# Kernel tuning notes

Hardware: AMD Instinct MI355X
Metric: run time of the kernel (lower is better)

## Reference

```python
import jax, jax.numpy as jnp
import numpy as np

LOG2_HASHMAP_SIZE = 19
HASHTABLE_SIZE = 2 ** LOG2_HASHMAP_SIZE
FEATURES_PER_LEVEL = 2
RES = 128
N_POINTS = 4194304

# Instant-NGP spatial hash primes (prime0 = 1)
_P1 = jnp.uint32(2654435761)
_P2 = jnp.uint32(805459861)


def _hash3(ix, iy, iz):
    # uint32 wrap-around multiply/xor matches torch int32 overflow bit pattern;
    # modulus is a power of two, so uint32 mod == floored int32 mod low bits.
    h = ix.astype(jnp.uint32) ^ (iy.astype(jnp.uint32) * _P1) ^ (iz.astype(jnp.uint32) * _P2)
    return (h % jnp.uint32(HASHTABLE_SIZE)).astype(jnp.int32)


def setup_inputs() -> dict:
    key = jax.random.key(0)
    kx, kt = jax.random.split(key)
    x = jax.random.uniform(kx, (N_POINTS, 3), dtype=jnp.float32)
    # hashtable = rand*2-1, scaled by hashmap_scale (=1)
    hashtable = jax.random.uniform(kt, (HASHTABLE_SIZE, FEATURES_PER_LEVEL), dtype=jnp.float32) * 2.0 - 1.0
    return {"x": x, "hashtable": hashtable}


def reference(x, hashtable):
    xr = x.reshape(-1, 3)
    x_scaled = xr * RES
    xf = jnp.floor(x_scaled).astype(jnp.int32)   # [N,3]
    xc = jnp.ceil(x_scaled).astype(jnp.int32)    # [N,3]

    fx, fy, fz = xf[:, 0], xf[:, 1], xf[:, 2]
    cx, cy, cz = xc[:, 0], xc[:, 1], xc[:, 2]

    # 8 corner hashes, ordering matches (h0..h7) = (000,100,010,001,110,101,011,111)
    h000 = _hash3(fx, fy, fz)
    h100 = _hash3(cx, fy, fz)
    h010 = _hash3(fx, cy, fz)
    h001 = _hash3(fx, fy, cz)
    h110 = _hash3(cx, cy, fz)
    h101 = _hash3(cx, fy, cz)
    h011 = _hash3(fx, cy, cz)
    h111 = _hash3(cx, cy, cz)

    idx = jnp.stack([h000, h100, h010, h001, h110, h101, h011, h111], axis=0)  # [8,N]
    v = hashtable[idx]  # [8, N, F] scattered gather
    v000, v100, v010, v001, v110, v101, v011, v111 = v

    d = x_scaled - xf.astype(x_scaled.dtype)  # [N,3] fractional offsets
    dx = d[:, 0:1]
    dy = d[:, 1:2]
    dz = d[:, 2:3]

    c00 = v000 * (1 - dx) + v100 * dx
    c01 = v001 * (1 - dx) + v101 * dx
    c10 = v010 * (1 - dx) + v110 * dx
    c11 = v011 * (1 - dx) + v111 * dx
    c0 = c00 * (1 - dy) + c10 * dy
    c1 = c01 * (1 - dy) + c11 * dy
    out = c0 * (1 - dz) + c1 * dz  # [N, F]

    return out.reshape(x.shape[:-1] + (FEATURES_PER_LEVEL,))
```

## Files before the change

kernel.cpp:

```cpp
#include <hip/hip_runtime.h>
#include <stdint.h>

#define LOG2_HASHMAP_SIZE 19
#define HASHTABLE_SIZE (1u << LOG2_HASHMAP_SIZE)
#define HASHTABLE_MASK (HASHTABLE_SIZE - 1u)
#define RES_F 128.0f

typedef float f32x2 __attribute__((ext_vector_type(2)));
typedef float f32x4 __attribute__((ext_vector_type(4)));
typedef uint32_t u32x4 __attribute__((ext_vector_type(4)));
typedef int i32x4 __attribute__((ext_vector_type(4)));

__device__ u32x4 llvm_amdgcn_raw_buffer_load_v4u32(i32x4 rsrc, int voffset,
                                                   int soffset, int aux)
    __asm("llvm.amdgcn.raw.buffer.load.v4i32");
__device__ uint32_t llvm_amdgcn_raw_buffer_load_u32(i32x4 rsrc, int voffset,
                                                    int soffset, int aux)
    __asm("llvm.amdgcn.raw.buffer.load.i32");

__device__ __forceinline__ i32x4 make_srd(const void* p, uint32_t bytes) {
    union { const void* p; uint32_t u[2]; } a;
    a.p = p;
    i32x4 r;
    r.x = (int)a.u[0];
    r.y = (int)(a.u[1] & 0xFFFFu);
    r.z = (int)bytes;
    r.w = 0x00020000;
    return r;
}

__device__ __forceinline__ float bf16w_lo(uint32_t w) {
    return __uint_as_float(w << 16);
}
__device__ __forceinline__ float bf16w_hi(uint32_t w) {
    return __uint_as_float(w & 0xFFFF0000u);
}

__device__ __forceinline__ uint32_t sel4(u32x4 q, uint32_t e) {
    uint32_t lo = (e & 1u) ? q.y : q.x;
    uint32_t hi = (e & 1u) ? q.w : q.z;
    return (e & 2u) ? hi : lo;
}

__device__ __forceinline__ uint32_t pack_bf16x2(float a, float b) {
    uint32_t ua = __float_as_uint(a);
    uint32_t ub = __float_as_uint(b);
    ua = ua + 0x7FFFu + ((ua >> 16) & 1u);
    ub = ub + 0x7FFFu + ((ub >> 16) & 1u);
    return (ua >> 16) | (ub & 0xFFFF0000u);
}

__global__ __launch_bounds__(256) void convert_table_kernel(
    const f32x4* __restrict__ table4,
    u32x4* __restrict__ ws4)
{
    int i = blockIdx.x * blockDim.x + threadIdx.x;
    f32x4 e01 = table4[2 * i + 0];
    f32x4 e23 = table4[2 * i + 1];
    u32x4 o;
    o.x = pack_bf16x2(e01.x, e01.y);
    o.y = pack_bf16x2(e01.z, e01.w);
    o.z = pack_bf16x2(e23.x, e23.y);
    o.w = pack_bf16x2(e23.z, e23.w);
    ws4[i] = o;
}


struct Gen {
    u32x4 q[4];
    uint32_t w1[4];
    uint32_t i0[4];
    uint32_t mm;
    float dx, dy, dz;
};

__device__ __forceinline__ Gen issue_point(const float* __restrict__ x,
                                           i32x4 srd, int p) {
    Gen g;
    float xs = __builtin_nontemporal_load(x + 3 * p + 0) * RES_F;
    float ys = __builtin_nontemporal_load(x + 3 * p + 1) * RES_F;
    float zs = __builtin_nontemporal_load(x + 3 * p + 2) * RES_F;
    float fxf = floorf(xs), fyf = floorf(ys), fzf = floorf(zs);
    int fx = (int)fxf, fy = (int)fyf, fz = (int)fzf;
    int cx = (int)ceilf(xs), cy = (int)ceilf(ys), cz = (int)ceilf(zs);
    g.dx = xs - fxf;
    g.dy = ys - fyf;
    g.dz = zs - fzf;

    uint32_t ufx = (uint32_t)fx;
    g.mm = ufx ^ (uint32_t)cx;
    uint32_t fyp = (uint32_t)fy * 2654435761u;
    uint32_t cyp = (uint32_t)cy * 2654435761u;
    uint32_t fzp = (uint32_t)fz * 805459861u;
    uint32_t czp = (uint32_t)cz * 805459861u;

    g.i0[0] = (ufx ^ fyp ^ fzp) & HASHTABLE_MASK;
    g.i0[1] = (ufx ^ cyp ^ fzp) & HASHTABLE_MASK;
    g.i0[2] = (ufx ^ fyp ^ czp) & HASHTABLE_MASK;
    g.i0[3] = (ufx ^ cyp ^ czp) & HASHTABLE_MASK;

    #pragma unroll
    for (int j = 0; j < 4; ++j) {
        g.q[j] = llvm_amdgcn_raw_buffer_load_v4u32(
            srd, (int)((g.i0[j] << 2) & ~15u), 0, 0);
    }
    if (g.mm > 3u) {
        #pragma unroll
        for (int j = 0; j < 4; ++j) {
            g.w1[j] = llvm_amdgcn_raw_buffer_load_u32(
                srd, (int)((g.i0[j] ^ g.mm) << 2), 0, 0);
        }
    }
    return g;
}

__device__ __forceinline__ f32x2 consume_point(const Gen& g) {
    uint32_t w0[4], w1[4];
    #pragma unroll
    for (int j = 0; j < 4; ++j) {
        uint32_t e0 = g.i0[j] & 3u;
        w0[j] = sel4(g.q[j], e0);
        w1[j] = (g.mm <= 3u) ? sel4(g.q[j], e0 ^ g.mm) : g.w1[j];
    }

    float dx = g.dx, dy = g.dy, dz = g.dz;
    float wx = 1.0f - dx, wy = 1.0f - dy, wz = 1.0f - dz;

    float c00x = bf16w_lo(w0[0]) * wx + bf16w_lo(w1[0]) * dx;
    float c00y = bf16w_hi(w0[0]) * wx + bf16w_hi(w1[0]) * dx;
    float c10x = bf16w_lo(w0[1]) * wx + bf16w_lo(w1[1]) * dx;
    float c10y = bf16w_hi(w0[1]) * wx + bf16w_hi(w1[1]) * dx;
    float c01x = bf16w_lo(w0[2]) * wx + bf16w_lo(w1[2]) * dx;
    float c01y = bf16w_hi(w0[2]) * wx + bf16w_hi(w1[2]) * dx;
    float c11x = bf16w_lo(w0[3]) * wx + bf16w_lo(w1[3]) * dx;
    float c11y = bf16w_hi(w0[3]) * wx + bf16w_hi(w1[3]) * dx;

    float c0x = c00x * wy + c10x * dy;
    float c0y = c00y * wy + c10y * dy;
    float c1x = c01x * wy + c11x * dy;
    float c1y = c01y * wy + c11y * dy;

    f32x2 r;
    r.x = c0x * wz + c1x * dz;
    r.y = c0y * wz + c1y * dz;
    return r;
}

__device__ __forceinline__ void store_out(f32x2* __restrict__ out, int p,
                                          f32x2 v) {
    __builtin_nontemporal_store(v, out + p);
}

__global__ __launch_bounds__(256) void featurefield_pipe_kernel(
    const float* __restrict__ x,
    const uint32_t* __restrict__ tb,
    f32x2* __restrict__ out,
    int NT)
{
    int t = blockIdx.x * blockDim.x + threadIdx.x;
    if (t >= NT) return;

    i32x4 srd = make_srd(tb, HASHTABLE_SIZE * 4u);

    Gen g0 = issue_point(x, srd, t);
    Gen g1 = issue_point(x, srd, t + NT);
    store_out(out, t, consume_point(g0));
    Gen g2 = issue_point(x, srd, t + 2 * NT);
    store_out(out, t + NT, consume_point(g1));
    Gen g3 = issue_point(x, srd, t + 3 * NT);
    store_out(out, t + 2 * NT, consume_point(g2));
    store_out(out, t + 3 * NT, consume_point(g3));
}

__global__ __launch_bounds__(256) void featurefield_fp32_kernel(
    const float* __restrict__ x,
    const float2* __restrict__ table,
    f32x2* __restrict__ out,
    int n_points)
{
    int p = blockIdx.x * blockDim.x + threadIdx.x;
    if (p >= n_points) return;

    float xs = x[3 * p + 0] * RES_F;
    float ys = x[3 * p + 1] * RES_F;
    float zs = x[3 * p + 2] * RES_F;
    float fxf = floorf(xs), fyf = floorf(ys), fzf = floorf(zs);
    int fx = (int)fxf, fy = (int)fyf, fz = (int)fzf;
    int cx = (int)ceilf(xs), cy = (int)ceilf(ys), cz = (int)ceilf(zs);
    float dx = xs - fxf, dy = ys - fyf, dz = zs - fzf;
    uint32_t ufx = (uint32_t)fx, ucx = (uint32_t)cx;
    uint32_t fyp = (uint32_t)fy * 2654435761u, cyp = (uint32_t)cy * 2654435761u;
    uint32_t fzp = (uint32_t)fz * 805459861u, czp = (uint32_t)cz * 805459861u;
    uint32_t h0 = (ufx ^ fyp ^ fzp) & HASHTABLE_MASK;
    uint32_t h1 = (ucx ^ fyp ^ fzp) & HASHTABLE_MASK;
    uint32_t h2 = (ufx ^ cyp ^ fzp) & HASHTABLE_MASK;
    uint32_t h3 = (ufx ^ fyp ^ czp) & HASHTABLE_MASK;
    uint32_t h4 = (ucx ^ cyp ^ fzp) & HASHTABLE_MASK;
    uint32_t h5 = (ucx ^ fyp ^ czp) & HASHTABLE_MASK;
    uint32_t h6 = (ufx ^ cyp ^ czp) & HASHTABLE_MASK;
    uint32_t h7 = (ucx ^ cyp ^ czp) & HASHTABLE_MASK;

    float2 v0 = table[h0], v1 = table[h1], v2 = table[h2], v3 = table[h3];
    float2 v4 = table[h4], v5 = table[h5], v6 = table[h6], v7 = table[h7];

    float wx = 1.0f - dx, wy = 1.0f - dy, wz = 1.0f - dz;
    float c00x = v0.x * wx + v1.x * dx, c00y = v0.y * wx + v1.y * dx;
    float c01x = v3.x * wx + v5.x * dx, c01y = v3.y * wx + v5.y * dx;
    float c10x = v2.x * wx + v4.x * dx, c10y = v2.y * wx + v4.y * dx;
    float c11x = v6.x * wx + v7.x * dx, c11y = v6.y * wx + v7.y * dx;
    float c0x = c00x * wy + c10x * dy, c0y = c00y * wy + c10y * dy;
    float c1x = c01x * wy + c11x * dy, c1y = c01y * wy + c11y * dy;

    f32x2 r;
    r.x = c0x * wz + c1x * dz;
    r.y = c0y * wz + c1y * dz;
    __builtin_nontemporal_store(r, out + p);
}

extern "C" void kernel_launch(void* const* d_in, const int* in_sizes, int n_in,
                              void* d_out, int out_size, void* d_ws, size_t ws_size,
                              hipStream_t stream) {
    const float* x = (const float*)d_in[0];
    f32x2* out = (f32x2*)d_out;

    int n_points = in_sizes[0] / 3;
    size_t need = (size_t)HASHTABLE_SIZE * 4u;

    if (ws_size >= need && (n_points & 3) == 0) {
        const f32x4* table4 = (const f32x4*)d_in[1];
        u32x4* ws4 = (u32x4*)d_ws;
        int conv_threads = HASHTABLE_SIZE / 4;
        convert_table_kernel<<<conv_threads / 256, 256, 0, stream>>>(table4, ws4);

        int NT = n_points / 4;
        int grid = (NT + 255) / 256;
        featurefield_pipe_kernel<<<grid, 256, 0, stream>>>(
            x, (const uint32_t*)d_ws, out, NT);
    } else {
        const float2* table = (const float2*)d_in[1];
        int grid = (n_points + 255) / 256;
        featurefield_fp32_kernel<<<grid, 256, 0, stream>>>(x, table, out, n_points);
    }
}
```

Baseline: 179.8 us.

## Compact divergent far-corner gathers through an LDS queue per block

Replaces the four-points-per-thread software-pipelined kernel with one point per thread. The 'far' corner loads, needed when the x-corner is outside the 16-byte vector, are queued in shared memory via an atomic counter. All threads then issue those loads densely, so lane divergence is avoided. This adds three block barriers and LDS traffic, and removes the cross-point latency overlap the previous pipelined kernel provided.

```diff
diff --git a/kernel.cpp b/kernel.cpp
--- a/kernel.cpp
+++ b/kernel.cpp
@@ -65,65 +65,82 @@
     ws4[i] = o;
 }
 
-
-struct Gen {
-    u32x4 q[4];
-    uint32_t w1[4];
-    uint32_t i0[4];
-    uint32_t mm;
-    float dx, dy, dz;
-};
-
-__device__ __forceinline__ Gen issue_point(const float* __restrict__ x,
-                                           i32x4 srd, int p) {
-    Gen g;
+__global__ __launch_bounds__(256) void featurefield_cmp_kernel(
+    const float* __restrict__ x,
+    const uint32_t* __restrict__ tb,
+    f32x2* __restrict__ out,
+    int n_points)
+{
+    __shared__ uint32_t s_queue[1024];
+    __shared__ uint32_t s_res[1024];
+    __shared__ uint32_t s_cnt;
+
+    int tid = threadIdx.x;
+    int p = blockIdx.x * blockDim.x + tid;
+
+    if (tid == 0) s_cnt = 0;
+
+    i32x4 srd = make_srd(tb, HASHTABLE_SIZE * 4u);
+
     float xs = __builtin_nontemporal_load(x + 3 * p + 0) * RES_F;
     float ys = __builtin_nontemporal_load(x + 3 * p + 1) * RES_F;
     float zs = __builtin_nontemporal_load(x + 3 * p + 2) * RES_F;
+
     float fxf = floorf(xs), fyf = floorf(ys), fzf = floorf(zs);
     int fx = (int)fxf, fy = (int)fyf, fz = (int)fzf;
     int cx = (int)ceilf(xs), cy = (int)ceilf(ys), cz = (int)ceilf(zs);
-    g.dx = xs - fxf;
-    g.dy = ys - fyf;
-    g.dz = zs - fzf;
+    float dx = xs - fxf, dy = ys - fyf, dz = zs - fzf;
 
     uint32_t ufx = (uint32_t)fx;
-    g.mm = ufx ^ (uint32_t)cx;
+    uint32_t mm = ufx ^ (uint32_t)cx;
     uint32_t fyp = (uint32_t)fy * 2654435761u;
     uint32_t cyp = (uint32_t)cy * 2654435761u;
     uint32_t fzp = (uint32_t)fz * 805459861u;
     uint32_t czp = (uint32_t)cz * 805459861u;
 
-    g.i0[0] = (ufx ^ fyp ^ fzp) & HASHTABLE_MASK;
-    g.i0[1] = (ufx ^ cyp ^ fzp) & HASHTABLE_MASK;
-    g.i0[2] = (ufx ^ fyp ^ czp) & HASHTABLE_MASK;
-    g.i0[3] = (ufx ^ cyp ^ czp) & HASHTABLE_MASK;
-
+    uint32_t i0[4];
+    i0[0] = (ufx ^ fyp ^ fzp) & HASHTABLE_MASK;
+    i0[1] = (ufx ^ cyp ^ fzp) & HASHTABLE_MASK;
+    i0[2] = (ufx ^ fyp ^ czp) & HASHTABLE_MASK;
+    i0[3] = (ufx ^ cyp ^ czp) & HASHTABLE_MASK;
+
+    u32x4 q[4];
     #pragma unroll
     for (int j = 0; j < 4; ++j) {
-        g.q[j] = llvm_amdgcn_raw_buffer_load_v4u32(
-            srd, (int)((g.i0[j] << 2) & ~15u), 0, 0);
-    }
-    if (g.mm > 3u) {
+        q[j] = llvm_amdgcn_raw_buffer_load_v4u32(
+            srd, (int)((i0[j] << 2) & ~15u), 0, 0);
+    }
+
+    __syncthreads();
+
+    uint32_t base = 0;
+    bool far = (mm > 3u);
+    if (far) {
+        base = atomicAdd(&s_cnt, 4u);
         #pragma unroll
         for (int j = 0; j < 4; ++j) {
-            g.w1[j] = llvm_amdgcn_raw_buffer_load_u32(
-                srd, (int)((g.i0[j] ^ g.mm) << 2), 0, 0);
+            s_queue[base + j] = (i0[j] ^ mm);
         }
     }
-    return g;
-}
-
-__device__ __forceinline__ f32x2 consume_point(const Gen& g) {
+
+    __syncthreads();
+
+    uint32_t Q = s_cnt;
+    for (uint32_t i = tid; i < Q; i += 256u) {
+        uint32_t idx = s_queue[i];
+        s_res[i] = llvm_amdgcn_raw_buffer_load_u32(srd, (int)(idx << 2), 0, 0);
+    }
+
+    __syncthreads();
+
     uint32_t w0[4], w1[4];
     #pragma unroll
     for (int j = 0; j < 4; ++j) {
-        uint32_t e0 = g.i0[j] & 3u;
-        w0[j] = sel4(g.q[j], e0);
-        w1[j] = (g.mm <= 3u) ? sel4(g.q[j], e0 ^ g.mm) : g.w1[j];
-    }
-
-    float dx = g.dx, dy = g.dy, dz = g.dz;
+        uint32_t e0 = i0[j] & 3u;
+        w0[j] = sel4(q[j], e0);
+        w1[j] = far ? s_res[base + j] : sel4(q[j], e0 ^ mm);
+    }
+
     float wx = 1.0f - dx, wy = 1.0f - dy, wz = 1.0f - dz;
 
     float c00x = bf16w_lo(w0[0]) * wx + bf16w_lo(w1[0]) * dx;
@@ -143,33 +160,7 @@
     f32x2 r;
     r.x = c0x * wz + c1x * dz;
     r.y = c0y * wz + c1y * dz;
-    return r;
-}
-
-__device__ __forceinline__ void store_out(f32x2* __restrict__ out, int p,
-                                          f32x2 v) {
-    __builtin_nontemporal_store(v, out + p);
-}
-
-__global__ __launch_bounds__(256) void featurefield_pipe_kernel(
-    const float* __restrict__ x,
-    const uint32_t* __restrict__ tb,
-    f32x2* __restrict__ out,
-    int NT)
-{
-    int t = blockIdx.x * blockDim.x + threadIdx.x;
-    if (t >= NT) return;
-
-    i32x4 srd = make_srd(tb, HASHTABLE_SIZE * 4u);
-
-    Gen g0 = issue_point(x, srd, t);
-    Gen g1 = issue_point(x, srd, t + NT);
-    store_out(out, t, consume_point(g0));
-    Gen g2 = issue_point(x, srd, t + 2 * NT);
-    store_out(out, t + NT, consume_point(g1));
-    Gen g3 = issue_point(x, srd, t + 3 * NT);
-    store_out(out, t + 2 * NT, consume_point(g2));
-    store_out(out, t + 3 * NT, consume_point(g3));
+    __builtin_nontemporal_store(r, out + p);
 }
 
 __global__ __launch_bounds__(256) void featurefield_fp32_kernel(
@@ -226,16 +217,15 @@
     int n_points = in_sizes[0] / 3;
     size_t need = (size_t)HASHTABLE_SIZE * 4u;
 
-    if (ws_size >= need && (n_points & 3) == 0) {
+    if (ws_size >= need && (n_points & 255) == 0) {
         const f32x4* table4 = (const f32x4*)d_in[1];
         u32x4* ws4 = (u32x4*)d_ws;
         int conv_threads = HASHTABLE_SIZE / 4;
         convert_table_kernel<<<conv_threads / 256, 256, 0, stream>>>(table4, ws4);
 
-        int NT = n_points / 4;
-        int grid = (NT + 255) / 256;
-        featurefield_pipe_kernel<<<grid, 256, 0, stream>>>(
-            x, (const uint32_t*)d_ws, out, NT);
+        int grid = n_points / 256;
+        featurefield_cmp_kernel<<<grid, 256, 0, stream>>>(
+            x, (const uint32_t*)d_ws, out, n_points);
     } else {
         const float2* table = (const float2*)d_in[1];
         int grid = (n_points + 255) / 256;
```

New measurement: 176.3 us. No clear change (-2.0%).
